# Kernel tuning notes

Hardware: AMD Instinct MI355X
Metric: run time of the kernel (lower is better)

Reference implementation:

```python
import jax, jax.numpy as jnp
import numpy as np

NHEAD = 16
D_MODEL = 1024
SCALE = 1.0 / np.sqrt(D_MODEL // NHEAD)
DROP_P = 0.2


def setup_inputs() -> dict:
    key = jax.random.key(0)
    kq, kk, kv = jax.random.split(key, 3)
    B, S, H, E = 2, 2048, NHEAD, D_MODEL // NHEAD
    q = jax.random.normal(kq, (B, S, H, E), dtype=jnp.float32)
    k = jax.random.normal(kk, (B, S, H, E), dtype=jnp.float32)
    v = jax.random.normal(kv, (B, S, H, E), dtype=jnp.float32)
    return {"q": q, "k": k, "v": v}


def reference(q, k, v):
    # scores: [B, H, L, S]
    scores = jnp.einsum('blhe,bshe->bhls', q, k)
    attn = jax.nn.softmax(SCALE * scores, axis=-1)
    # dropout p=0.2 (training mode), fixed key -> deterministic reference
    dkey = jax.random.key(42)
    keep = jax.random.bernoulli(dkey, 1.0 - DROP_P, attn.shape)
    attn_weights = jnp.where(keep, attn / (1.0 - DROP_P), 0.0).astype(attn.dtype)
    context = jnp.einsum('bhls,bshd->blhd', attn_weights, v)
    return (context, attn_weights)
```

## Files before the change

### kernel.cpp

```cpp
#include <hip/hip_runtime.h>
#include <stdint.h>

#define NHEAD 16
#define SEQ 2048
#define KEEP_THR 0xCCCCCE00u
#define CTX_ELEMS 4194304
#define QS 0.18033688f

typedef __attribute__((ext_vector_type(8))) short bf16x8;
typedef __attribute__((ext_vector_type(4))) float f32x4;
typedef __attribute__((ext_vector_type(4))) unsigned short u16x4;

__device__ __forceinline__ unsigned short bfs(float f) {
  uint32_t x = __float_as_uint(f);
  return (unsigned short)((x + 0x7FFFu + ((x >> 16) & 1u)) >> 16);
}

__device__ __forceinline__ u16x4 cvt4(f32x4 v) {
  u16x4 p;
  p[0] = bfs(v[0]); p[1] = bfs(v[1]); p[2] = bfs(v[2]); p[3] = bfs(v[3]);
  return p;
}

__device__ __forceinline__ void tf2x32(uint32_t x0, uint32_t x1,
                                       uint32_t& o0, uint32_t& o1) {
  const uint32_t K1 = 42u;
  const uint32_t K2 = 0x1BD11BDAu ^ 42u;
  x1 += K1;
#define TFR(r) { x0 += x1; x1 = __builtin_rotateleft32(x1, r); x1 ^= x0; }
  TFR(13) TFR(15) TFR(26) TFR(6)
  x0 += K1; x1 += K2 + 1u;
  TFR(17) TFR(29) TFR(16) TFR(24)
  x0 += K2; x1 += 2u;
  TFR(13) TFR(15) TFR(26) TFR(6)
  x1 += K1 + 3u;
  TFR(17) TFR(29) TFR(16) TFR(24)
  x0 += K1; x1 += K2 + 4u;
  TFR(13) TFR(15) TFR(26) TFR(6)
  x0 += K2; x1 += 5u;
#undef TFR
  o0 = x0; o1 = x1;
}

__global__ __launch_bounds__(512, 8) void sdpa_kernel(
    const float* __restrict__ Q, const float* __restrict__ Kg,
    const float* __restrict__ Vg, float* __restrict__ outC,
    float* __restrict__ outA) {

  __shared__ __align__(16) char ldsKV[16384];
  __shared__ __align__(16) char ldsW[10240];
  __shared__ float red[2][64];

  const int tid = (int)threadIdx.x;
  const int w = tid >> 6, lane = tid & 63;
  const int wr = w >> 1, wc = w & 1;
  const int c = lane & 15, g = lane >> 4;

  const int bid = (int)blockIdx.x;
  const int swz = (bid & 7) * 128 + (bid >> 3);
  const int bh = swz >> 5;
  const int b = bh >> 4, h = bh & 15;
  const int lbase = (swz & 31) << 6;

  const int ssl = tid >> 4;
  const int se0 = (tid & 15) << 2;
  int kwb = (ssl << 7) + (se0 << 1); kwb ^= (ssl & 7) << 4;
  const int kgo = ssl * 1024 + se0;
  int vwb0[4], vwb1[4];
#pragma unroll
  for (int i = 0; i < 4; ++i) {
    const int e = se0 + i;
    const int x = (((e >> 2) & 7) ^ ((e & 3) << 1)) << 4;
    vwb0[i] = (8192 + (e << 7) + (ssl << 1)) ^ x;
    vwb1[i] = (8192 + (e << 7) + ((ssl + 32) << 1)) ^ x;
  }
  const int sl0f = (wc << 5) + c;
  const int fx = (sl0f & 7) << 4;
  const int fbA = ((sl0f << 7) + (g << 4)) ^ fx;
  const int fbB = ((sl0f << 7) + 64 + (g << 4)) ^ fx;
  const int wwb = w * 1280 + ((g << 2) * 80) + (c << 1);
  const int wrb = w * 1280 + c * 80 + (g << 4);
  int pvb[4];
  {
    const int s0v = (wc << 5) + (g << 3);
#pragma unroll
    for (int e4 = 0; e4 < 4; ++e4) {
      const int e = (e4 << 4) + c;
      int byte = 8192 + (e << 7) + (s0v << 1);
      byte ^= ((((e >> 2) & 7) ^ ((e & 3) << 1)) << 4);
      pvb[e4] = byte;
    }
  }

  bf16x8 qf[2];
  {
    const int lA = lbase + (wr << 4) + c;
    const float* p = Q + (((size_t)(b * SEQ + lA) * NHEAD + h) << 6) + (g << 3);
#pragma unroll
    for (int kh = 0; kh < 2; ++kh) {
      f32x4 x = *(const f32x4*)(p + (kh << 5));
      f32x4 y = *(const f32x4*)(p + (kh << 5) + 4);
      bf16x8 f;
      f[0] = (short)bfs(x[0] * QS); f[1] = (short)bfs(x[1] * QS);
      f[2] = (short)bfs(x[2] * QS); f[3] = (short)bfs(x[3] * QS);
      f[4] = (short)bfs(y[0] * QS); f[5] = (short)bfs(y[1] * QS);
      f[6] = (short)bfs(y[2] * QS); f[7] = (short)bfs(y[3] * QS);
      qf[kh] = f;
    }
  }

  const float* kbase = Kg + (((size_t)b * SEQ * NHEAD + h) << 6);
  const float* vbase = Vg + (((size_t)b * SEQ * NHEAD + h) << 6);

  float rs[4] = {0.f, 0.f, 0.f, 0.f};
  f32x4 kra = *(const f32x4*)(kbase + kgo);
  f32x4 krb = *(const f32x4*)(kbase + kgo + 32768);

#pragma unroll 1
  for (int t = 0; t < 32; ++t) {
    __syncthreads();
    *(u16x4*)(ldsKV + kwb) = cvt4(kra);
    *(u16x4*)(ldsKV + kwb + 4096) = cvt4(krb);
    if (t < 31) {
      const int nf = (t + 1) << 6;
      kra = *(const f32x4*)(kbase + (size_t)nf * 1024 + kgo);
      krb = *(const f32x4*)(kbase + (size_t)nf * 1024 + kgo + 32768);
    }
    __syncthreads();

    bf16x8 kf00 = *(const bf16x8*)(ldsKV + fbA);
    bf16x8 kf01 = *(const bf16x8*)(ldsKV + fbA + 2048);
    bf16x8 kf10 = *(const bf16x8*)(ldsKV + fbB);
    bf16x8 kf11 = *(const bf16x8*)(ldsKV + fbB + 2048);
    f32x4 sc0 = {0.f, 0.f, 0.f, 0.f}, sc1 = {0.f, 0.f, 0.f, 0.f};
    sc0 = __builtin_amdgcn_mfma_f32_16x16x32_bf16(qf[0], kf00, sc0, 0, 0, 0);
    sc1 = __builtin_amdgcn_mfma_f32_16x16x32_bf16(qf[0], kf01, sc1, 0, 0, 0);
    sc0 = __builtin_amdgcn_mfma_f32_16x16x32_bf16(qf[1], kf10, sc0, 0, 0, 0);
    sc1 = __builtin_amdgcn_mfma_f32_16x16x32_bf16(qf[1], kf11, sc1, 0, 0, 0);
#pragma unroll
    for (int r = 0; r < 4; ++r)
      rs[r] += __builtin_amdgcn_exp2f(sc0[r]) + __builtin_amdgcn_exp2f(sc1[r]);
  }

#pragma unroll
  for (int r = 0; r < 4; ++r) {
#pragma unroll
    for (int d = 1; d < 16; d <<= 1) rs[r] += __shfl_xor(rs[r], d);
  }
  if (c == 0) {
#pragma unroll
    for (int r = 0; r < 4; ++r)
      red[wc][(wr << 4) + (g << 2) + r] = rs[r];
  }
  kra = *(const f32x4*)(kbase + kgo);
  krb = *(const f32x4*)(kbase + kgo + 32768);
  f32x4 vra = *(const f32x4*)(vbase + kgo);
  f32x4 vrb = *(const f32x4*)(vbase + kgo + 32768);
  __syncthreads();
  float I[4];
#pragma unroll
  for (int r = 0; r < 4; ++r)
    I[r] = 1.25f / (rs[r] + red[1 - wc][(wr << 4) + (g << 2) + r]);

  f32x4 ctx[4];
#pragma unroll
  for (int e4 = 0; e4 < 4; ++e4) ctx[e4] = (f32x4){0.f, 0.f, 0.f, 0.f};

  const uint32_t nbase =
      ((uint32_t)(bh * SEQ + lbase + (wr << 4) + (g << 2)) << 11) |
      (uint32_t)((wc << 5) + c);
  float* const pa0 = outA + nbase;

#pragma unroll 1
  for (int t = 0; t < 32; ++t) {
    const int sbase = t << 6;
    __syncthreads();
    *(u16x4*)(ldsKV + kwb) = cvt4(kra);
    *(u16x4*)(ldsKV + kwb + 4096) = cvt4(krb);
#pragma unroll
    for (int i = 0; i < 4; ++i) {
      *(unsigned short*)(ldsKV + vwb0[i]) = bfs(vra[i]);
      *(unsigned short*)(ldsKV + vwb1[i]) = bfs(vrb[i]);
    }
    if (t < 31) {
      const int nf = (t + 1) << 6;
      kra = *(const f32x4*)(kbase + (size_t)nf * 1024 + kgo);
      krb = *(const f32x4*)(kbase + (size_t)nf * 1024 + kgo + 32768);
      vra = *(const f32x4*)(vbase + (size_t)nf * 1024 + kgo);
      vrb = *(const f32x4*)(vbase + (size_t)nf * 1024 + kgo + 32768);
    }
    __syncthreads();

    bf16x8 kf00 = *(const bf16x8*)(ldsKV + fbA);
    bf16x8 kf01 = *(const bf16x8*)(ldsKV + fbA + 2048);
    bf16x8 kf10 = *(const bf16x8*)(ldsKV + fbB);
    bf16x8 kf11 = *(const bf16x8*)(ldsKV + fbB + 2048);
    f32x4 sc0 = {0.f, 0.f, 0.f, 0.f}, sc1 = {0.f, 0.f, 0.f, 0.f};
    sc0 = __builtin_amdgcn_mfma_f32_16x16x32_bf16(qf[0], kf00, sc0, 0, 0, 0);
    sc1 = __builtin_amdgcn_mfma_f32_16x16x32_bf16(qf[0], kf01, sc1, 0, 0, 0);
    sc0 = __builtin_amdgcn_mfma_f32_16x16x32_bf16(qf[1], kf10, sc0, 0, 0, 0);
    sc1 = __builtin_amdgcn_mfma_f32_16x16x32_bf16(qf[1], kf11, sc1, 0, 0, 0);

#pragma unroll
    for (int ct = 0; ct < 2; ++ct) {
#pragma unroll
      for (int r = 0; r < 4; ++r) {
        const float pv = __builtin_amdgcn_exp2f(ct ? sc1[r] : sc0[r]) * I[r];
        const uint32_t noff = (uint32_t)((r << 11) + sbase + (ct << 4));
        uint32_t o0, o1;
        tf2x32(0u, nbase + noff, o0, o1);
        const float wv = ((o0 ^ o1) < KEEP_THR) ? pv : 0.f;
        __builtin_nontemporal_store(wv, pa0 + noff);
        *(unsigned short*)(ldsW + wwb + r * 80 + (ct << 5)) = bfs(wv);
      }
    }
    bf16x8 af = *(const bf16x8*)(ldsW + wrb);
#pragma unroll
    for (int e4 = 0; e4 < 4; ++e4) {
      bf16x8 vf = *(const bf16x8*)(ldsKV + pvb[e4]);
      ctx[e4] = __builtin_amdgcn_mfma_f32_16x16x32_bf16(af, vf, ctx[e4], 0, 0, 0);
    }
  }

  __syncthreads();
  float* ex = (float*)ldsKV;
  if (wc == 1) {
#pragma unroll
    for (int e4 = 0; e4 < 4; ++e4)
#pragma unroll
      for (int r = 0; r < 4; ++r)
        ex[((wr << 4) + (g << 2) + r) * 64 + (e4 << 4) + c] = ctx[e4][r];
  }
  __syncthreads();
  if (wc == 0) {
#pragma unroll
    for (int e4 = 0; e4 < 4; ++e4)
#pragma unroll
      for (int r = 0; r < 4; ++r) {
        const int l = lbase + (wr << 4) + (g << 2) + r;
        const int e = (e4 << 4) + c;
        outC[(((size_t)(b * SEQ + l) * NHEAD + h) << 6) + e] =
            ctx[e4][r] + ex[((wr << 4) + (g << 2) + r) * 64 + (e4 << 4) + c];
      }
  }
}

extern "C" void kernel_launch(void* const* d_in, const int* in_sizes, int n_in,
                              void* d_out, int out_size, void* d_ws, size_t ws_size,
                              hipStream_t stream) {
  (void)in_sizes; (void)n_in; (void)out_size; (void)d_ws; (void)ws_size;
  const float* q = (const float*)d_in[0];
  const float* k = (const float*)d_in[1];
  const float* v = (const float*)d_in[2];
  float* outC = (float*)d_out;
  float* outA = outC + CTX_ELEMS;
  sdpa_kernel<<<dim3(1024), dim3(512), 0, stream>>>(q, k, v, outC, outA);
}
```

Baseline: 440.6 us.

## Double-buffer K/V shared-memory tiles to drop one barrier per iteration

Doubles the K/V LDS staging area and alternates between two buffers in both the row-sum pass and the output pass. The next tile is written into the idle buffer while the current one is read, so the second __syncthreads per iteration goes away. Global loads are prefetched two tiles ahead, with prologue stores placed before each loop. The trade-off is that LDS per block grows from about 27 KB to about 43 KB, which may lower how many blocks fit on a CU.

```diff
diff --git a/kernel.cpp b/kernel.cpp
--- a/kernel.cpp
+++ b/kernel.cpp
@@ -47,7 +47,7 @@
     const float* __restrict__ Vg, float* __restrict__ outC,
     float* __restrict__ outA) {
 
-  __shared__ __align__(16) char ldsKV[16384];
+  __shared__ __align__(16) char ldsKV[32768];
   __shared__ __align__(16) char ldsW[10240];
   __shared__ float red[2][64];
 
@@ -115,23 +115,29 @@
   float rs[4] = {0.f, 0.f, 0.f, 0.f};
   f32x4 kra = *(const f32x4*)(kbase + kgo);
   f32x4 krb = *(const f32x4*)(kbase + kgo + 32768);
+  *(u16x4*)(ldsKV + kwb) = cvt4(kra);
+  *(u16x4*)(ldsKV + kwb + 4096) = cvt4(krb);
+  kra = *(const f32x4*)(kbase + 65536 + kgo);
+  krb = *(const f32x4*)(kbase + 65536 + kgo + 32768);
 
 #pragma unroll 1
   for (int t = 0; t < 32; ++t) {
     __syncthreads();
-    *(u16x4*)(ldsKV + kwb) = cvt4(kra);
-    *(u16x4*)(ldsKV + kwb + 4096) = cvt4(krb);
+    char* nbp = ldsKV + (((t + 1) & 1) << 14);
     if (t < 31) {
-      const int nf = (t + 1) << 6;
-      kra = *(const f32x4*)(kbase + (size_t)nf * 1024 + kgo);
-      krb = *(const f32x4*)(kbase + (size_t)nf * 1024 + kgo + 32768);
-    }
-    __syncthreads();
-
-    bf16x8 kf00 = *(const bf16x8*)(ldsKV + fbA);
-    bf16x8 kf01 = *(const bf16x8*)(ldsKV + fbA + 2048);
-    bf16x8 kf10 = *(const bf16x8*)(ldsKV + fbB);
-    bf16x8 kf11 = *(const bf16x8*)(ldsKV + fbB + 2048);
+      *(u16x4*)(nbp + kwb) = cvt4(kra);
+      *(u16x4*)(nbp + kwb + 4096) = cvt4(krb);
+    }
+    if (t < 30) {
+      const size_t go = ((size_t)(t + 2) << 16) + kgo;
+      kra = *(const f32x4*)(kbase + go);
+      krb = *(const f32x4*)(kbase + go + 32768);
+    }
+    char* bp = ldsKV + ((t & 1) << 14);
+    bf16x8 kf00 = *(const bf16x8*)(bp + fbA);
+    bf16x8 kf01 = *(const bf16x8*)(bp + fbA + 2048);
+    bf16x8 kf10 = *(const bf16x8*)(bp + fbB);
+    bf16x8 kf11 = *(const bf16x8*)(bp + fbB + 2048);
     f32x4 sc0 = {0.f, 0.f, 0.f, 0.f}, sc1 = {0.f, 0.f, 0.f, 0.f};
     sc0 = __builtin_amdgcn_mfma_f32_16x16x32_bf16(qf[0], kf00, sc0, 0, 0, 0);
     sc1 = __builtin_amdgcn_mfma_f32_16x16x32_bf16(qf[0], kf01, sc1, 0, 0, 0);
@@ -171,30 +177,45 @@
       (uint32_t)((wc << 5) + c);
   float* const pa0 = outA + nbase;
 
+  *(u16x4*)(ldsKV + kwb) = cvt4(kra);
+  *(u16x4*)(ldsKV + kwb + 4096) = cvt4(krb);
+#pragma unroll
+  for (int i = 0; i < 4; ++i) {
+    *(unsigned short*)(ldsKV + vwb0[i]) = bfs(vra[i]);
+    *(unsigned short*)(ldsKV + vwb1[i]) = bfs(vrb[i]);
+  }
+  kra = *(const f32x4*)(kbase + 65536 + kgo);
+  krb = *(const f32x4*)(kbase + 65536 + kgo + 32768);
+  vra = *(const f32x4*)(vbase + 65536 + kgo);
+  vrb = *(const f32x4*)(vbase + 65536 + kgo + 32768);
+
 #pragma unroll 1
   for (int t = 0; t < 32; ++t) {
     const int sbase = t << 6;
     __syncthreads();
-    *(u16x4*)(ldsKV + kwb) = cvt4(kra);
-    *(u16x4*)(ldsKV + kwb + 4096) = cvt4(krb);
-#pragma unroll
-    for (int i = 0; i < 4; ++i) {
-      *(unsigned short*)(ldsKV + vwb0[i]) = bfs(vra[i]);
-      *(unsigned short*)(ldsKV + vwb1[i]) = bfs(vrb[i]);
-    }
+    char* nbp = ldsKV + (((t + 1) & 1) << 14);
     if (t < 31) {
-      const int nf = (t + 1) << 6;
-      kra = *(const f32x4*)(kbase + (size_t)nf * 1024 + kgo);
-      krb = *(const f32x4*)(kbase + (size_t)nf * 1024 + kgo + 32768);
-      vra = *(const f32x4*)(vbase + (size_t)nf * 1024 + kgo);
-      vrb = *(const f32x4*)(vbase + (size_t)nf * 1024 + kgo + 32768);
-    }
-    __syncthreads();
-
-    bf16x8 kf00 = *(const bf16x8*)(ldsKV + fbA);
-    bf16x8 kf01 = *(const bf16x8*)(ldsKV + fbA + 2048);
-    bf16x8 kf10 = *(const bf16x8*)(ldsKV + fbB);
-    bf16x8 kf11 = *(const bf16x8*)(ldsKV + fbB + 2048);
+      *(u16x4*)(nbp + kwb) = cvt4(kra);
+      *(u16x4*)(nbp + kwb + 4096) = cvt4(krb);
+#pragma unroll
+      for (int i = 0; i < 4; ++i) {
+        *(unsigned short*)(nbp + vwb0[i]) = bfs(vra[i]);
+        *(unsigned short*)(nbp + vwb1[i]) = bfs(vrb[i]);
+      }
+    }
+    if (t < 30) {
+      const size_t go = ((size_t)(t + 2) << 16) + kgo;
+      kra = *(const f32x4*)(kbase + go);
+      krb = *(const f32x4*)(kbase + go + 32768);
+      vra = *(const f32x4*)(vbase + go);
+      vrb = *(const f32x4*)(vbase + go + 32768);
+    }
+    char* bp = ldsKV + ((t & 1) << 14);
+
+    bf16x8 kf00 = *(const bf16x8*)(bp + fbA);
+    bf16x8 kf01 = *(const bf16x8*)(bp + fbA + 2048);
+    bf16x8 kf10 = *(const bf16x8*)(bp + fbB);
+    bf16x8 kf11 = *(const bf16x8*)(bp + fbB + 2048);
     f32x4 sc0 = {0.f, 0.f, 0.f, 0.f}, sc1 = {0.f, 0.f, 0.f, 0.f};
     sc0 = __builtin_amdgcn_mfma_f32_16x16x32_bf16(qf[0], kf00, sc0, 0, 0, 0);
     sc1 = __builtin_amdgcn_mfma_f32_16x16x32_bf16(qf[0], kf01, sc1, 0, 0, 0);
@@ -217,7 +238,7 @@
     bf16x8 af = *(const bf16x8*)(ldsW + wrb);
 #pragma unroll
     for (int e4 = 0; e4 < 4; ++e4) {
-      bf16x8 vf = *(const bf16x8*)(ldsKV + pvb[e4]);
+      bf16x8 vf = *(const bf16x8*)(bp + pvb[e4]);
       ctx[e4] = __builtin_amdgcn_mfma_f32_16x16x32_bf16(af, vf, ctx[e4], 0, 0, 0);
     }
   }
```

New measurement: 404.1 us. 8.3% less time.
